# Kernel optimization log

Measured on AMD Instinct MI355X. Metric: run time of the kernel, lower is better.

Reference implementation:

```python
import jax, jax.numpy as jnp
import numpy as np

START_TAG = 2
STOP_TAG = 3
NEG = -10000.0


def _lstm_dir(x, w_ih, w_hh, b_ih, b_hh, h0, c0):
    """Single-direction LSTM over x:[T,F]. PyTorch gate order i,f,g,o."""
    xp = x @ w_ih.T + b_ih  # [T, 4H] - big GEMM done once

    def step(carry, xt):
        h, c = carry
        g = xt + h @ w_hh.T + b_hh
        i, f, gg, o = jnp.split(g, 4)
        c = jax.nn.sigmoid(f) * c + jax.nn.sigmoid(i) * jnp.tanh(gg)
        h = jax.nn.sigmoid(o) * jnp.tanh(c)
        return (h, c), h

    _, hs = jax.lax.scan(step, (h0, c0), xp)
    return hs  # [T, H]


def _viterbi(feats, transitions):
    # feats: [T, n_tags]; transitions[next, prev]
    n = transitions.shape[0]
    init = jnp.full((n,), NEG, feats.dtype).at[START_TAG].set(0.0)

    def step(fv, feat):
        scores = fv[None, :] + transitions          # [next, prev]
        bptr = jnp.argmax(scores, axis=1)           # best prev per next
        return jnp.max(scores, axis=1) + feat, bptr

    fv, bptrs = jax.lax.scan(step, init, feats)
    terminal = fv + transitions[STOP_TAG]
    best = jnp.argmax(terminal)
    score = terminal[best]

    def back(tag, bp):
        return bp[tag], tag  # emit tag at step t, carry tag at t-1

    _, path = jax.lax.scan(back, best, bptrs, reverse=True)
    return score, path  # scalar, [T] int32


def setup_inputs() -> dict:
    key = jax.random.key(0)
    T, F, H = 4096, 1024, 2048
    H2 = H // 2
    NTAG = 4
    ks = jax.random.split(key, 16)
    s_ih = 1.0 / np.sqrt(H2)

    def u(k, shape, s):
        return jax.random.uniform(k, shape, jnp.float32, -s, s)

    transitions = jax.random.normal(ks[13], (NTAG, NTAG), jnp.float32)
    transitions = transitions.at[START_TAG, :].set(NEG)
    transitions = transitions.at[:, STOP_TAG].set(NEG)

    return {
        "sentence": jax.random.normal(ks[0], (T, F), jnp.float32),
        "h0": jax.random.normal(ks[1], (2, 1, H2), jnp.float32),
        "c0": jax.random.normal(ks[2], (2, 1, H2), jnp.float32),
        "w_ih_f": u(ks[3], (4 * H2, F), s_ih),
        "w_hh_f": u(ks[4], (4 * H2, H2), s_ih),
        "b_ih_f": u(ks[5], (4 * H2,), s_ih),
        "b_hh_f": u(ks[6], (4 * H2,), s_ih),
        "w_ih_b": u(ks[7], (4 * H2, F), s_ih),
        "w_hh_b": u(ks[8], (4 * H2, H2), s_ih),
        "b_ih_b": u(ks[9], (4 * H2,), s_ih),
        "b_hh_b": u(ks[10], (4 * H2,), s_ih),
        "w_tag": u(ks[11], (NTAG, H), 1.0 / np.sqrt(H)),
        "b_tag": u(ks[12], (NTAG,), 1.0 / np.sqrt(H)),
        "transitions": transitions,
    }


def reference(sentence, h0, c0, w_ih_f, w_hh_f, b_ih_f, b_hh_f,
              w_ih_b, w_hh_b, b_ih_b, b_hh_b, w_tag, b_tag, transitions):
    # Bidirectional LSTM, batch=1 (torch stacks directions on dim 0 of h0/c0)
    h_fwd = _lstm_dir(sentence, w_ih_f, w_hh_f, b_ih_f, b_hh_f, h0[0, 0], c0[0, 0])
    h_bwd = _lstm_dir(sentence[::-1], w_ih_b, w_hh_b, b_ih_b, b_hh_b, h0[1, 0], c0[1, 0])[::-1]
    lstm_out = jnp.concatenate([h_fwd, h_bwd], axis=-1)  # [T, hidden_dim]
    feats = lstm_out @ w_tag.T + b_tag                    # [T, 4]
    score, path = _viterbi(feats, transitions)
    return score, path
```

## Files before the change

### kernel.cpp

```cpp
#include <hip/hip_runtime.h>
#include <cstddef>
#include <cstdint>

#define T_LEN 4096
#define FDIM  1024
#define H2DIM 1024
#define GDIM  4096

#define NEGV (-10000.0f)
#define START_TAG 2
#define STOP_TAG 3

#define XP_OFF      ((size_t)0)
#define XP_BYTES    ((size_t)2 * T_LEN * GDIM * 4)
#define HIST_OFF    (XP_OFF + XP_BYTES)
#define HIST_BYTES  ((size_t)T_LEN * 2048 * 4)
#define FEATS_OFF   (HIST_OFF + HIST_BYTES)
#define FEATS_BYTES ((size_t)T_LEN * 4 * 4)
#define SLOTS_OFF   (FEATS_OFF + FEATS_BYTES)
#define SLOTS_BYTES ((size_t)2 * 2 * 1024 * 8)
#define WS_NEED     (SLOTS_OFF + SLOTS_BYTES)

#define XB_OFF      (HIST_OFF)
#define WBF_OFF     (HIST_OFF + (size_t)8  * 1024 * 1024)
#define WBB_OFF     (HIST_OFF + (size_t)16 * 1024 * 1024)

__device__ __forceinline__ float sigm(float x) { return 1.0f / (1.0f + expf(-x)); }

__device__ __forceinline__ unsigned short f2bf(float f) {
    unsigned u = __float_as_uint(f);
    return (unsigned short)((u + 0x7FFFu + ((u >> 16) & 1u)) >> 16);
}

typedef short  bf16x8 __attribute__((ext_vector_type(8)));
typedef float  f32x4  __attribute__((ext_vector_type(4)));

__global__ __launch_bounds__(256)
void conv_bf16(const float* __restrict__ src, unsigned short* __restrict__ dst, int n4)
{
    int i = blockIdx.x * 256 + threadIdx.x;
    const int stride = gridDim.x * 256;
    for (; i < n4; i += stride) {
        const float4 v = ((const float4*)src)[i];
        ushort4 o;
        o.x = f2bf(v.x); o.y = f2bf(v.y); o.z = f2bf(v.z); o.w = f2bf(v.w);
        ((ushort4*)dst)[i] = o;
    }
}

__global__ __launch_bounds__(64)
void xp_gemm_mfma(const unsigned short* __restrict__ xb,
                  const unsigned short* __restrict__ wb_f,
                  const unsigned short* __restrict__ wb_b,
                  const float* __restrict__ bi_f, const float* __restrict__ bh_f,
                  const float* __restrict__ bi_b, const float* __restrict__ bh_b,
                  float* __restrict__ xp)
{
    const int lane = threadIdx.x;
    const int j0   = blockIdx.x * 64;
    const int t0   = blockIdx.y * 64;
    const int dir  = blockIdx.z;
    const unsigned short* __restrict__ wb = dir ? wb_b : wb_f;
    const float* __restrict__ bi = dir ? bi_b : bi_f;
    const float* __restrict__ bh = dir ? bh_b : bh_f;

    const int r  = lane & 15;
    const int kg = lane >> 4;

    const unsigned short* arow[4];
    const unsigned short* brow[4];
    #pragma unroll
    for (int s = 0; s < 4; ++s) {
        const int tg = t0 + s * 16 + r;
        const int sr = dir ? (T_LEN - 1 - tg) : tg;
        arow[s] = xb + (size_t)sr * FDIM + kg * 8;
        brow[s] = wb + (size_t)(j0 + s * 16 + r) * FDIM + kg * 8;
    }

    f32x4 acc[4][4];
    #pragma unroll
    for (int sm = 0; sm < 4; ++sm)
        #pragma unroll
        for (int sn = 0; sn < 4; ++sn)
            acc[sm][sn] = (f32x4){0.f, 0.f, 0.f, 0.f};

    for (int k0 = 0; k0 < FDIM; k0 += 32) {
        bf16x8 a[4], b[4];
        #pragma unroll
        for (int s = 0; s < 4; ++s) {
            a[s] = *(const bf16x8*)(arow[s] + k0);
            b[s] = *(const bf16x8*)(brow[s] + k0);
        }
        #pragma unroll
        for (int sm = 0; sm < 4; ++sm)
            #pragma unroll
            for (int sn = 0; sn < 4; ++sn)
                acc[sm][sn] = __builtin_amdgcn_mfma_f32_16x16x32_bf16(
                                  a[sm], b[sn], acc[sm][sn], 0, 0, 0);
    }

    float* __restrict__ xpd = xp + (size_t)dir * T_LEN * GDIM;
    #pragma unroll
    for (int sn = 0; sn < 4; ++sn) {
        const int col  = j0 + sn * 16 + r;
        const float bv = bi[col] + bh[col];
        #pragma unroll
        for (int sm = 0; sm < 4; ++sm) {
            #pragma unroll
            for (int j = 0; j < 4; ++j) {
                const int row = t0 + sm * 16 + kg * 4 + j;
                xpd[(size_t)row * GDIM + col] = acc[sm][sn][j] + bv;
            }
        }
    }
}

__global__ __launch_bounds__(256, 1)
void lstm_scan(const float* __restrict__ xp,
               const float* __restrict__ h0,
               const float* __restrict__ c0,
               const float* __restrict__ whh_f,
               const float* __restrict__ whh_b,
               float* __restrict__ hist,
               unsigned long long* __restrict__ slots)
{
    __shared__ float wsl[32][1024];
    __shared__ float hbuf[1024];
    __shared__ float gsh[32];

    const int tid = threadIdx.x;
    const int b   = blockIdx.x;
    const int dir = b >> 7;
    const int bi  = b & 127;
    const int u0  = bi * 8;
    const int rg  = tid >> 5;
    const int kc  = tid & 31;
    const int lrb = rg * 4;

    const float* __restrict__ whh = dir ? whh_b : whh_f;
    const size_t xpbase = (size_t)dir * T_LEN * GDIM;

    for (int lr = 0; lr < 32; ++lr) {
        const int grow = ((lr >> 3) << 10) + u0 + (lr & 7);
        *(float4*)&wsl[lr][tid * 4] = *(const float4*)&whh[(size_t)grow * H2DIM + tid * 4];
    }
    *(float4*)&hbuf[tid * 4] = *(const float4*)&h0[dir * H2DIM + tid * 4];
    float creg = 0.f;
    if (tid < 8) creg = c0[dir * H2DIM + u0 + tid];

    int grows[4];
    #pragma unroll
    for (int j = 0; j < 4; ++j) {
        const int lr = lrb + j;
        grows[j] = ((lr >> 3) << 10) + u0 + (lr & 7);
    }
    float xpc[4] = {0.f, 0.f, 0.f, 0.f};
    if (kc == 0) {
        #pragma unroll
        for (int j = 0; j < 4; ++j) xpc[j] = xp[xpbase + grows[j]];
    }
    __syncthreads();

    int budget = 4000000;

    for (int t = 0; t < T_LEN; ++t) {
        float xpn[4] = {0.f, 0.f, 0.f, 0.f};
        const int tnx = (t + 1 < T_LEN) ? (t + 1) : t;
        if (kc == 0) {
            #pragma unroll
            for (int j = 0; j < 4; ++j) xpn[j] = xp[xpbase + (size_t)tnx * GDIM + grows[j]];
        }

        float p0 = 0.f, p1 = 0.f, p2 = 0.f, p3 = 0.f;
        #pragma unroll
        for (int s = 0; s < 8; ++s) {
            const int ko = s * 128 + kc * 4;
            const float4 hv = *(const float4*)&hbuf[ko];
            const float4 w0 = *(const float4*)&wsl[lrb + 0][ko];
            const float4 w1 = *(const float4*)&wsl[lrb + 1][ko];
            const float4 w2 = *(const float4*)&wsl[lrb + 2][ko];
            const float4 w3 = *(const float4*)&wsl[lrb + 3][ko];
            p0 += w0.x*hv.x + w0.y*hv.y + w0.z*hv.z + w0.w*hv.w;
            p1 += w1.x*hv.x + w1.y*hv.y + w1.z*hv.z + w1.w*hv.w;
            p2 += w2.x*hv.x + w2.y*hv.y + w2.z*hv.z + w2.w*hv.w;
            p3 += w3.x*hv.x + w3.y*hv.y + w3.z*hv.z + w3.w*hv.w;
        }
        #pragma unroll
        for (int m = 16; m >= 1; m >>= 1) {
            p0 += __shfl_xor(p0, m);
            p1 += __shfl_xor(p1, m);
            p2 += __shfl_xor(p2, m);
            p3 += __shfl_xor(p3, m);
        }
        if (kc == 0) {
            gsh[lrb + 0] = p0 + xpc[0];
            gsh[lrb + 1] = p1 + xpc[1];
            gsh[lrb + 2] = p2 + xpc[2];
            gsh[lrb + 3] = p3 + xpc[3];
        }
        __syncthreads();

        if (tid < 8) {
            const float gi = gsh[tid];
            const float gf = gsh[8 + tid];
            const float gg = gsh[16 + tid];
            const float go = gsh[24 + tid];
            const float c  = sigm(gf) * creg + sigm(gi) * tanhf(gg);
            const float h  = sigm(go) * tanhf(c);
            creg = c;
            const int tg = dir ? (T_LEN - 1 - t) : t;
            hist[(size_t)tg * 2048 + dir * H2DIM + u0 + tid] = h;
            const unsigned long long pack =
                ((unsigned long long)(unsigned)(t + 1) << 32) |
                (unsigned long long)__float_as_uint(h);
            __hip_atomic_store(&slots[((size_t)((t + 1) & 1) * 2 + dir) * H2DIM + u0 + tid],
                               pack, __ATOMIC_RELAXED, __HIP_MEMORY_SCOPE_AGENT);
        }

        if (t + 1 < T_LEN) {
            const unsigned want = (unsigned)(t + 1);
            unsigned long long* sb = &slots[((size_t)((t + 1) & 1) * 2 + dir) * H2DIM + tid * 4];
            unsigned long long v0 = 0, v1 = 0, v2 = 0, v3 = 0;
            bool g0 = false, g1 = false, g2 = false, g3 = false;
            for (;;) {
                if (!g0) v0 = __hip_atomic_load(&sb[0], __ATOMIC_RELAXED, __HIP_MEMORY_SCOPE_AGENT);
                if (!g1) v1 = __hip_atomic_load(&sb[1], __ATOMIC_RELAXED, __HIP_MEMORY_SCOPE_AGENT);
                if (!g2) v2 = __hip_atomic_load(&sb[2], __ATOMIC_RELAXED, __HIP_MEMORY_SCOPE_AGENT);
                if (!g3) v3 = __hip_atomic_load(&sb[3], __ATOMIC_RELAXED, __HIP_MEMORY_SCOPE_AGENT);
                g0 = g0 || ((unsigned)(v0 >> 32) == want);
                g1 = g1 || ((unsigned)(v1 >> 32) == want);
                g2 = g2 || ((unsigned)(v2 >> 32) == want);
                g3 = g3 || ((unsigned)(v3 >> 32) == want);
                if (g0 && g1 && g2 && g3) break;
                if (--budget <= 0) break;
                __builtin_amdgcn_s_sleep(1);
            }
            float4 hv;
            hv.x = __uint_as_float((unsigned)v0);
            hv.y = __uint_as_float((unsigned)v1);
            hv.z = __uint_as_float((unsigned)v2);
            hv.w = __uint_as_float((unsigned)v3);
            *(float4*)&hbuf[tid * 4] = hv;
        }
        __syncthreads();
        if (kc == 0) { xpc[0] = xpn[0]; xpc[1] = xpn[1]; xpc[2] = xpn[2]; xpc[3] = xpn[3]; }
    }
}

__global__ __launch_bounds__(256)
void feats_kernel(const float* __restrict__ hist,
                  const float* __restrict__ w_tag,
                  const float* __restrict__ b_tag,
                  float* __restrict__ feats)
{
    const int t = blockIdx.x;
    const int tid = threadIdx.x;
    const float* __restrict__ hrow = hist + (size_t)t * 2048 + tid * 8;
    const float4 ha = *(const float4*)&hrow[0];
    const float4 hb = *(const float4*)&hrow[4];
    float p[4];
    #pragma unroll
    for (int n = 0; n < 4; ++n) {
        const float* __restrict__ wr = w_tag + n * 2048 + tid * 8;
        const float4 wa = *(const float4*)&wr[0];
        const float4 wb = *(const float4*)&wr[4];
        p[n] = ha.x*wa.x + ha.y*wa.y + ha.z*wa.z + ha.w*wa.w
             + hb.x*wb.x + hb.y*wb.y + hb.z*wb.z + hb.w*wb.w;
    }
    #pragma unroll
    for (int m = 32; m >= 1; m >>= 1) {
        #pragma unroll
        for (int n = 0; n < 4; ++n) p[n] += __shfl_down(p[n], m);
    }
    __shared__ float red[4][4];
    const int wv = tid >> 6;
    if ((tid & 63) == 0) {
        #pragma unroll
        for (int n = 0; n < 4; ++n) red[n][wv] = p[n];
    }
    __syncthreads();
    if (tid < 4)
        feats[(size_t)t * 4 + tid] = red[tid][0] + red[tid][1] + red[tid][2] + red[tid][3] + b_tag[tid];
}

__global__ __launch_bounds__(256)
void viterbi_kernel(const float* __restrict__ feats,
                    const float* __restrict__ trans,
                    float* __restrict__ out)
{
    __shared__ float fsh[T_LEN * 4];
    __shared__ unsigned bp[T_LEN];
    const int tid = threadIdx.x;
    for (int i = tid; i < T_LEN; i += 256)
        *(float4*)&fsh[i * 4] = *(const float4*)&feats[(size_t)i * 4];
    __syncthreads();
    if (tid == 0) {
        float tr[16];
        #pragma unroll
        for (int i = 0; i < 16; ++i) tr[i] = trans[i];
        float fv[4] = {NEGV, NEGV, NEGV, NEGV};
        fv[START_TAG] = 0.0f;
        for (int t = 0; t < T_LEN; ++t) {
            float nf[4]; unsigned pb = 0;
            #pragma unroll
            for (int n = 0; n < 4; ++n) {
                float m = fv[0] + tr[n * 4 + 0]; int bsel = 0;
                #pragma unroll
                for (int p = 1; p < 4; ++p) {
                    const float s = fv[p] + tr[n * 4 + p];
                    if (s > m) { m = s; bsel = p; }
                }
                nf[n] = m + fsh[t * 4 + n];
                pb |= (unsigned)bsel << (8 * n);
            }
            bp[t] = pb;
            fv[0] = nf[0]; fv[1] = nf[1]; fv[2] = nf[2]; fv[3] = nf[3];
        }
        float bm = fv[0] + tr[STOP_TAG * 4 + 0]; int best = 0;
        #pragma unroll
        for (int p = 1; p < 4; ++p) {
            const float s = fv[p] + tr[STOP_TAG * 4 + p];
            if (s > bm) { bm = s; best = p; }
        }
        out[0] = bm;
        int cur = best;
        for (int t = T_LEN - 1; t >= 0; --t) {
            out[1 + t] = (float)cur;
            cur = (int)((bp[t] >> (8 * cur)) & 0xffu);
        }
    }
}

extern "C" void kernel_launch(void* const* d_in, const int* in_sizes, int n_in,
                              void* d_out, int out_size, void* d_ws, size_t ws_size,
                              hipStream_t stream) {
    const float* x      = (const float*)d_in[0];
    const float* h0     = (const float*)d_in[1];
    const float* c0     = (const float*)d_in[2];
    const float* w_ih_f = (const float*)d_in[3];
    const float* w_hh_f = (const float*)d_in[4];
    const float* b_ih_f = (const float*)d_in[5];
    const float* b_hh_f = (const float*)d_in[6];
    const float* w_ih_b = (const float*)d_in[7];
    const float* w_hh_b = (const float*)d_in[8];
    const float* b_ih_b = (const float*)d_in[9];
    const float* b_hh_b = (const float*)d_in[10];
    const float* w_tag  = (const float*)d_in[11];
    const float* b_tag  = (const float*)d_in[12];
    const float* trans  = (const float*)d_in[13];
    float* out = (float*)d_out;

    if (ws_size < WS_NEED) return;

    char* ws = (char*)d_ws;
    float* xp    = (float*)(ws + XP_OFF);
    float* hist  = (float*)(ws + HIST_OFF);
    float* feats = (float*)(ws + FEATS_OFF);
    unsigned long long* slots = (unsigned long long*)(ws + SLOTS_OFF);
    unsigned short* xb  = (unsigned short*)(ws + XB_OFF);
    unsigned short* wbf = (unsigned short*)(ws + WBF_OFF);
    unsigned short* wbb = (unsigned short*)(ws + WBB_OFF);

    hipMemsetAsync(slots, 0, SLOTS_BYTES, stream);

    const int n4 = (T_LEN * FDIM) / 4;
    conv_bf16<<<1024, 256, 0, stream>>>(x,      xb,  n4);
    conv_bf16<<<1024, 256, 0, stream>>>(w_ih_f, wbf, n4);
    conv_bf16<<<1024, 256, 0, stream>>>(w_ih_b, wbb, n4);

    xp_gemm_mfma<<<dim3(64, 64, 2), 64, 0, stream>>>(
        xb, wbf, wbb, b_ih_f, b_hh_f, b_ih_b, b_hh_b, xp);

    void* ka[] = { (void*)&xp, (void*)&h0, (void*)&c0, (void*)&w_hh_f, (void*)&w_hh_b,
                   (void*)&hist, (void*)&slots };
    hipLaunchCooperativeKernel((void*)lstm_scan, dim3(256), dim3(256), ka, 0, stream);

    feats_kernel<<<T_LEN, 256, 0, stream>>>(hist, w_tag, b_tag, feats);
    viterbi_kernel<<<1, 256, 0, stream>>>(feats, trans, out);
}
```

Measured before the change: 14.33 ms.

## Parallelize Viterbi backtrace via map composition and interleave LSTM block directions

The Viterbi backtrace is rewritten as a parallel prefix over composed backpointer maps: each thread composes 16 steps, one thread scans 256 chunk maps, then every thread emits its own path segment. This replaces a serial 4096-step loop with dependent shared-memory loads. The forward pass now reads emissions eight at a time as float4 vectors, and LSTM scan blocks are interleaved by direction (even blocks forward, odd backward) rather than split into halves, which changes how blocks land on compute units. The added barriers and the serial 256-step scan carry some overhead, and the Viterbi stage is small relative to the LSTM scan.

```diff
diff --git a/kernel.cpp b/kernel.cpp
--- a/kernel.cpp
+++ b/kernel.cpp
@@ -30,6 +30,17 @@
 __device__ __forceinline__ unsigned short f2bf(float f) {
     unsigned u = __float_as_uint(f);
     return (unsigned short)((u + 0x7FFFu + ((u >> 16) & 1u)) >> 16);
+}
+
+__device__ __forceinline__ unsigned compose4(unsigned A, unsigned B) {
+    unsigned r = 0;
+    #pragma unroll
+    for (int c = 0; c < 4; ++c) {
+        const unsigned b = (B >> (8 * c)) & 3u;
+        const unsigned a = (A >> (8 * b)) & 3u;
+        r |= a << (8 * c);
+    }
+    return r;
 }
 
 typedef short  bf16x8 __attribute__((ext_vector_type(8)));
@@ -130,8 +141,8 @@
 
     const int tid = threadIdx.x;
     const int b   = blockIdx.x;
-    const int dir = b >> 7;
-    const int bi  = b & 127;
+    const int dir = b & 1;
+    const int bi  = b >> 1;
     const int u0  = bi * 8;
     const int rg  = tid >> 5;
     const int kc  = tid & 31;
@@ -290,31 +301,42 @@
 {
     __shared__ float fsh[T_LEN * 4];
     __shared__ unsigned bp[T_LEN];
+    __shared__ unsigned lmap[256];
+    __shared__ unsigned smap[256];
+    __shared__ int bestsh;
     const int tid = threadIdx.x;
     for (int i = tid; i < T_LEN; i += 256)
         *(float4*)&fsh[i * 4] = *(const float4*)&feats[(size_t)i * 4];
     __syncthreads();
+
     if (tid == 0) {
         float tr[16];
         #pragma unroll
         for (int i = 0; i < 16; ++i) tr[i] = trans[i];
         float fv[4] = {NEGV, NEGV, NEGV, NEGV};
         fv[START_TAG] = 0.0f;
-        for (int t = 0; t < T_LEN; ++t) {
-            float nf[4]; unsigned pb = 0;
+        for (int t0 = 0; t0 < T_LEN; t0 += 8) {
+            float4 f8[8];
             #pragma unroll
-            for (int n = 0; n < 4; ++n) {
-                float m = fv[0] + tr[n * 4 + 0]; int bsel = 0;
+            for (int j = 0; j < 8; ++j) f8[j] = *(const float4*)&fsh[(t0 + j) * 4];
+            #pragma unroll
+            for (int j = 0; j < 8; ++j) {
+                const float ft[4] = {f8[j].x, f8[j].y, f8[j].z, f8[j].w};
+                float nf[4]; unsigned pb = 0;
                 #pragma unroll
-                for (int p = 1; p < 4; ++p) {
-                    const float s = fv[p] + tr[n * 4 + p];
-                    if (s > m) { m = s; bsel = p; }
+                for (int n = 0; n < 4; ++n) {
+                    float m = fv[0] + tr[n * 4 + 0]; int bsel = 0;
+                    #pragma unroll
+                    for (int p = 1; p < 4; ++p) {
+                        const float s = fv[p] + tr[n * 4 + p];
+                        if (s > m) { m = s; bsel = p; }
+                    }
+                    nf[n] = m + ft[n];
+                    pb |= (unsigned)bsel << (8 * n);
                 }
-                nf[n] = m + fsh[t * 4 + n];
-                pb |= (unsigned)bsel << (8 * n);
+                bp[t0 + j] = pb;
+                fv[0] = nf[0]; fv[1] = nf[1]; fv[2] = nf[2]; fv[3] = nf[3];
             }
-            bp[t] = pb;
-            fv[0] = nf[0]; fv[1] = nf[1]; fv[2] = nf[2]; fv[3] = nf[3];
         }
         float bm = fv[0] + tr[STOP_TAG * 4 + 0]; int best = 0;
         #pragma unroll
@@ -323,11 +345,26 @@
             if (s > bm) { bm = s; best = p; }
         }
         out[0] = bm;
-        int cur = best;
-        for (int t = T_LEN - 1; t >= 0; --t) {
-            out[1 + t] = (float)cur;
-            cur = (int)((bp[t] >> (8 * cur)) & 0xffu);
-        }
+        bestsh = best;
+    }
+    __syncthreads();
+
+    const int c0 = tid * 16;
+    unsigned L = bp[c0 + 15];
+    #pragma unroll
+    for (int j = 14; j >= 0; --j) L = compose4(bp[c0 + j], L);
+    lmap[tid] = L;
+    __syncthreads();
+    if (tid == 0) {
+        unsigned acc = 0x03020100u;
+        for (int i = 255; i >= 0; --i) { smap[i] = acc; acc = compose4(lmap[i], acc); }
+    }
+    __syncthreads();
+    unsigned carry = smap[tid];
+    const int best = bestsh;
+    for (int t = c0 + 15; t >= c0; --t) {
+        out[1 + t] = (float)((carry >> (8 * best)) & 3u);
+        carry = compose4(bp[t], carry);
     }
 }
 
```

Measured after the change: 14.01 ms. -2.2%, faster.
